# Optimization experiments

Measured on AMD Instinct MI355X. Metric: run time of the kernel, lower is better.

The kernel has to match this reference:

```python
import jax, jax.numpy as jnp
import numpy as np

N_NODES = 16384
N_EDGES = 98304
N_CAND = 1024
# GAT config from default __init__: heads=[8,8,1], features=[3,64,128,64]
LAYERS = [
    (3, 8, 64, True, True),      # (f_in, n_heads, f_out, concat, elu)
    (512, 8, 128, True, True),
    (1024, 1, 64, False, False),
]


def _gat_layer(x, src, tgt, W, a_src, a_tgt, b, skipW, nh, fo, concat, act):
    n = x.shape[0]
    proj = (x @ W).reshape(n, nh, fo)                 # [N, NH, F]
    s_src = jnp.einsum('nhf,hf->nh', proj, a_src)     # [N, NH]
    s_tgt = jnp.einsum('nhf,hf->nh', proj, a_tgt)
    e = jax.nn.leaky_relu(s_src[src] + s_tgt[tgt], 0.2)   # [E, NH]
    # numerically stable segment softmax over incoming edges of each target node
    e_max = jax.ops.segment_max(e, tgt, num_segments=n)
    ex = jnp.exp(e - jax.lax.stop_gradient(e_max)[tgt])
    denom = jax.ops.segment_sum(ex, tgt, num_segments=n)
    alpha = ex / (denom[tgt] + 1e-16)                 # [E, NH]
    agg = jax.ops.segment_sum(proj[src] * alpha[:, :, None], tgt, num_segments=n)
    out = agg + (x @ skipW).reshape(n, nh, fo)        # skip connection (projected)
    out = out.reshape(n, nh * fo) if concat else out.mean(axis=1)
    out = out + b
    return jax.nn.elu(out) if act else out


def setup_inputs() -> dict:
    key = jax.random.key(0)
    ks = iter(jax.random.split(key, 32))
    d = {}
    d['fea'] = jax.random.normal(next(ks), (N_NODES, 3), dtype=jnp.float32)
    d['edge_index'] = jax.random.randint(next(ks), (2, N_EDGES), 0, N_NODES, dtype=jnp.int32)
    d['candidates_id'] = jax.random.randint(next(ks), (N_CAND,), 0, N_NODES, dtype=jnp.int32)
    for i, (fi, nh, fo, concat, _) in enumerate(LAYERS):
        sc = 1.0 / np.sqrt(fi)
        d[f'W{i}'] = jax.random.normal(next(ks), (fi, nh * fo), dtype=jnp.float32) * sc
        d[f'a_src{i}'] = jax.random.normal(next(ks), (nh, fo), dtype=jnp.float32) * 0.1
        d[f'a_tgt{i}'] = jax.random.normal(next(ks), (nh, fo), dtype=jnp.float32) * 0.1
        d[f'b{i}'] = jnp.zeros((nh * fo if concat else fo,), dtype=jnp.float32)
        d[f'skip{i}'] = jax.random.normal(next(ks), (fi, nh * fo), dtype=jnp.float32) * sc
    # MLP head build_mlp(256, 3, 64, 1): 64->256 Tanh 256->256 Tanh 256->1
    for j, (a, bdim) in enumerate([(64, 256), (256, 256), (256, 1)], start=1):
        d[f'mW{j}'] = jax.random.normal(next(ks), (a, bdim), dtype=jnp.float32) / np.sqrt(a)
        d[f'mb{j}'] = jnp.zeros((bdim,), dtype=jnp.float32)
    return d


def reference(fea, edge_index, candidates_id,
              W0, a_src0, a_tgt0, b0, skip0,
              W1, a_src1, a_tgt1, b1, skip1,
              W2, a_src2, a_tgt2, b2, skip2,
              mW1, mb1, mW2, mb2, mW3, mb3):
    src, tgt = edge_index[0], edge_index[1]
    x = fea
    params = [(W0, a_src0, a_tgt0, b0, skip0), (W1, a_src1, a_tgt1, b1, skip1),
              (W2, a_src2, a_tgt2, b2, skip2)]
    for (fi, nh, fo, concat, act), (W, asr, atg, b, sk) in zip(LAYERS, params):
        x = _gat_layer(x, src, tgt, W, asr, atg, b, sk, nh, fo, concat, act)
    cand = x[candidates_id]                              # [C, 64]
    h = jnp.tanh(cand @ mW1 + mb1)
    h = jnp.tanh(h @ mW2 + mb2)
    prob = (h @ mW3 + mb3).squeeze(-1)                   # [C]
    return prob, candidates_id
```

## Files before the change

kernel.cpp:

```cpp
#include <hip/hip_runtime.h>
#include <cmath>

#define N_NODES 16384
#define N_EDGES 98304
#define N_CAND  1024

typedef __bf16 bf16x8 __attribute__((ext_vector_type(8)));
typedef short  s16x8  __attribute__((ext_vector_type(8)));
typedef float  f32x4  __attribute__((ext_vector_type(4)));
typedef unsigned short u16x2 __attribute__((ext_vector_type(2)));
typedef unsigned short u16x4 __attribute__((ext_vector_type(4)));

__device__ __forceinline__ unsigned short f2bf(float x) {
    unsigned u = __float_as_uint(x);
    return (unsigned short)((u + 0x7fffu + ((u >> 16) & 1u)) >> 16);
}
__device__ __forceinline__ float bf2f(unsigned short b) {
    return __uint_as_float((unsigned)b << 16);
}

#define GLL(gp, lp) __builtin_amdgcn_global_load_lds(                          \
    (const __attribute__((address_space(1))) unsigned int*)(const void*)(gp),  \
    (__attribute__((address_space(3))) unsigned int*)(void*)(lp), 16, 0, 0)

__global__ __launch_bounds__(256) void k_hist(const int* __restrict__ tgt,
                                              int* __restrict__ deg) {
    int e = blockIdx.x * 256 + threadIdx.x;
    if (e < N_EDGES) atomicAdd(&deg[tgt[e]], 1);
}

__global__ __launch_bounds__(256) void k_scan1(const int* __restrict__ deg,
                                               int* __restrict__ off,
                                               int* __restrict__ bsum) {
    __shared__ int s[256];
    int b = blockIdx.x, tid = threadIdx.x;
    int v = deg[b * 256 + tid];
    s[tid] = v;
    __syncthreads();
    for (int o = 1; o < 256; o <<= 1) {
        int t = (tid >= o) ? s[tid - o] : 0;
        __syncthreads();
        s[tid] += t;
        __syncthreads();
    }
    off[b * 256 + tid] = s[tid] - v;
    if (tid == 255) bsum[b] = s[255];
}

__global__ __launch_bounds__(64) void k_scan2(const int* __restrict__ bsum,
                                              int* __restrict__ bbase,
                                              int* __restrict__ off) {
    int tid = threadIdx.x;
    int v = bsum[tid];
    int x = v;
    #pragma unroll
    for (int o = 1; o < 64; o <<= 1) {
        int t = __shfl_up(x, o);
        if (tid >= o) x += t;
    }
    bbase[tid] = x - v;
    if (tid == 63) off[N_NODES] = x;
}

__global__ __launch_bounds__(256) void k_scan3(int* __restrict__ off,
                                               const int* __restrict__ bbase,
                                               int* __restrict__ cursor) {
    int i = blockIdx.x * 256 + threadIdx.x;
    int o = off[i] + bbase[blockIdx.x];
    off[i] = o;
    cursor[i] = o;
}

__global__ __launch_bounds__(256) void k_scatter(const int* __restrict__ ei,
                                                 int* __restrict__ cursor,
                                                 int* __restrict__ csrc) {
    int e = blockIdx.x * 256 + threadIdx.x;
    if (e < N_EDGES) {
        int s = ei[e];
        int t = ei[N_EDGES + e];
        int pos = atomicAdd(&cursor[t], 1);
        csrc[pos] = s;
    }
}

__global__ __launch_bounds__(256) void k_l0s(const float* __restrict__ fea,
                                             const float* __restrict__ W0,
                                             const float* __restrict__ as,
                                             const float* __restrict__ at,
                                             float* __restrict__ ssrc,
                                             float* __restrict__ stgt) {
    int n = blockIdx.x, tid = threadIdx.x;
    float f0 = fea[n * 3 + 0], f1 = fea[n * 3 + 1], f2 = fea[n * 3 + 2];
    int c1 = tid, c2 = tid + 256;
    float p1 = f0 * W0[c1] + f1 * W0[512 + c1] + f2 * W0[1024 + c1];
    float p2 = f0 * W0[c2] + f1 * W0[512 + c2] + f2 * W0[1024 + c2];
    float vs1 = p1 * as[c1], vt1 = p1 * at[c1];
    float vs2 = p2 * as[c2], vt2 = p2 * at[c2];
    #pragma unroll
    for (int o = 32; o; o >>= 1) {
        vs1 += __shfl_xor(vs1, o); vt1 += __shfl_xor(vt1, o);
        vs2 += __shfl_xor(vs2, o); vt2 += __shfl_xor(vt2, o);
    }
    int lane = tid & 63, w = tid >> 6;
    if (lane == 0) {
        ssrc[n * 8 + w]     = vs1;  stgt[n * 8 + w]     = vt1;
        ssrc[n * 8 + w + 4] = vs2;  stgt[n * 8 + w + 4] = vt2;
    }
}

template <int F, int NTOT>
__global__ __launch_bounds__(256) void k_pack(const float* __restrict__ src0,
                                              const float* __restrict__ src1,
                                              int splitN,
                                              unsigned short* __restrict__ hi,
                                              unsigned short* __restrict__ lo) {
    constexpr int NKB = F / 32;
    constexpr int TOT = (NTOT / 128) * NKB * 512;
    int s = blockIdx.x * 256 + threadIdx.x;
    if (s >= TOT) return;
    int nb = s / (NKB * 512);
    int rem = s - nb * (NKB * 512);
    int kb = rem >> 9;
    int sl = rem & 511;
    int c = sl >> 7, n = sl & 127;
    int col = nb * 128 + n;
    const float* src;
    int cc, stride;
    if (col < splitN) { src = src0; cc = col; stride = splitN; }
    else              { src = src1; cc = col - splitN; stride = NTOT - splitN; }
    int k0 = kb * 32 + c * 8;
    s16x8 hv, lv;
    #pragma unroll
    for (int j = 0; j < 8; ++j) {
        float w = src[(size_t)(k0 + j) * stride + cc];
        unsigned short h = f2bf(w);
        hv[j] = (short)h;
        lv[j] = (short)f2bf(w - bf2f(h));
    }
    *(s16x8*)(hi + (size_t)s * 8) = hv;
    *(s16x8*)(lo + (size_t)s * 8) = lv;
}

template <int F, int NTOT>
__global__ __launch_bounds__(256, 2) void k_gemm_mfma(
    const unsigned short* __restrict__ Xhi, const unsigned short* __restrict__ Xlo,
    const unsigned short* __restrict__ Wph, const unsigned short* __restrict__ Wpl,
    float* __restrict__ out0, float* __restrict__ out1, int splitN) {
    constexpr int NKB = F / 32;
    __shared__ unsigned short lds[2 * 16384];
    const int tid = threadIdx.x;
    const int bm  = blockIdx.y * 128;
    const int nb  = blockIdx.x;

    const int sA0 = tid, sA1 = tid + 256;
    const int rA0 = sA0 >> 2, rA1 = sA1 >> 2;
    const int cA0 = (sA0 & 3) ^ ((rA0 >> 1) & 3);
    const int cA1 = (sA1 & 3) ^ ((rA1 >> 1) & 3);
    const unsigned short* gAh0 = Xhi + (size_t)(bm + rA0) * F + cA0 * 8;
    const unsigned short* gAh1 = Xhi + (size_t)(bm + rA1) * F + cA1 * 8;
    const unsigned short* gAl0 = Xlo + (size_t)(bm + rA0) * F + cA0 * 8;
    const unsigned short* gAl1 = Xlo + (size_t)(bm + rA1) * F + cA1 * 8;
    const unsigned short* gBh  = Wph + (size_t)nb * NKB * 4096;
    const unsigned short* gBl  = Wpl + (size_t)nb * NKB * 4096;

    const int wave = tid >> 6, lane = tid & 63;
    const int wm = wave >> 1, wn = wave & 1;
    const int l15 = lane & 15, lc = lane >> 4;

    int offA[4], offB[4];
    #pragma unroll
    for (int mi = 0; mi < 4; ++mi) {
        int row = wm * 64 + mi * 16 + l15;
        int chp = lc ^ ((row >> 1) & 3);
        offA[mi] = row * 32 + chp * 8;
    }
    #pragma unroll
    for (int ni = 0; ni < 4; ++ni) {
        int n = wn * 64 + ni * 16 + l15;
        offB[ni] = 8192 + (lc * 128 + n) * 8;
    }

    f32x4 acc[4][4];
    #pragma unroll
    for (int i = 0; i < 4; ++i)
        #pragma unroll
        for (int j = 0; j < 4; ++j)
            acc[i][j] = (f32x4){0.f, 0.f, 0.f, 0.f};

    auto stage = [&](int kb, int buf) {
        unsigned short* l = &lds[buf * 16384];
        const size_t ka  = (size_t)kb * 32;
        const size_t kbb = (size_t)kb * 4096;
        GLL(gAh0 + ka, l + sA0 * 8);
        GLL(gAh1 + ka, l + sA1 * 8);
        GLL(gAl0 + ka, l + 4096 + sA0 * 8);
        GLL(gAl1 + ka, l + 4096 + sA1 * 8);
        GLL(gBh + kbb + sA0 * 8, l + 8192 + sA0 * 8);
        GLL(gBh + kbb + sA1 * 8, l + 8192 + sA1 * 8);
        GLL(gBl + kbb + sA0 * 8, l + 12288 + sA0 * 8);
        GLL(gBl + kbb + sA1 * 8, l + 12288 + sA1 * 8);
    };

    stage(0, 0);
    __syncthreads();

    for (int kb = 0; kb < NKB; ++kb) {
        const int buf = kb & 1;
        if (kb + 1 < NKB) stage(kb + 1, buf ^ 1);
        const unsigned short* l = &lds[buf * 16384];
        bf16x8 ah[4], al[4], bh[4], bl[4];
        #pragma unroll
        for (int mi = 0; mi < 4; ++mi) {
            ah[mi] = *(const bf16x8*)(l + offA[mi]);
            al[mi] = *(const bf16x8*)(l + 4096 + offA[mi]);
        }
        #pragma unroll
        for (int ni = 0; ni < 4; ++ni) {
            bh[ni] = *(const bf16x8*)(l + offB[ni]);
            bl[ni] = *(const bf16x8*)(l + 4096 + offB[ni]);
        }
        #pragma unroll
        for (int mi = 0; mi < 4; ++mi)
            #pragma unroll
            for (int ni = 0; ni < 4; ++ni) {
                acc[mi][ni] = __builtin_amdgcn_mfma_f32_16x16x32_bf16(ah[mi], bh[ni], acc[mi][ni], 0, 0, 0);
                acc[mi][ni] = __builtin_amdgcn_mfma_f32_16x16x32_bf16(ah[mi], bl[ni], acc[mi][ni], 0, 0, 0);
                acc[mi][ni] = __builtin_amdgcn_mfma_f32_16x16x32_bf16(al[mi], bh[ni], acc[mi][ni], 0, 0, 0);
            }
        __syncthreads();
    }

    #pragma unroll
    for (int ni = 0; ni < 4; ++ni) {
        int col = nb * 128 + wn * 64 + ni * 16 + l15;
        float* o;
        int cc, stride;
        if (col < splitN) { o = out0; cc = col; stride = splitN; }
        else              { o = out1; cc = col - splitN; stride = NTOT - splitN; }
        #pragma unroll
        for (int mi = 0; mi < 4; ++mi) {
            int row0 = bm + wm * 64 + mi * 16 + lc * 4;
            #pragma unroll
            for (int r = 0; r < 4; ++r)
                o[(size_t)(row0 + r) * stride + cc] = acc[mi][ni][r];
        }
    }
}

template <int H, int FO>
__global__ __launch_bounds__(256) void k_scores(const float* __restrict__ P,
                                                const float* __restrict__ asrc,
                                                const float* __restrict__ atgt,
                                                float* __restrict__ ssrc,
                                                float* __restrict__ stgt) {
    constexpr int K = H * FO;
    int gid  = blockIdx.x * 4 + (threadIdx.x >> 6);
    int lane = threadIdx.x & 63;
    int n = gid / H, h = gid - n * H;
    if (n >= N_NODES) return;
    float vs = 0.f, vt = 0.f;
    #pragma unroll
    for (int q = 0; q < FO / 64; ++q) {
        int f = lane + q * 64;
        float p = P[(size_t)n * K + h * FO + f];
        vs += p * asrc[h * FO + f];
        vt += p * atgt[h * FO + f];
    }
    #pragma unroll
    for (int o = 32; o; o >>= 1) {
        vs += __shfl_xor(vs, o);
        vt += __shfl_xor(vt, o);
    }
    if (lane == 0) {
        ssrc[n * H + h] = vs;
        stgt[n * H + h] = vt;
    }
}

__global__ __launch_bounds__(256) void k_attn0(
    const float* __restrict__ fea, const float* __restrict__ W0,
    const float* __restrict__ sk0, const float* __restrict__ ssrc,
    const float* __restrict__ stgt, const int* __restrict__ off,
    const int* __restrict__ csrc, const float* __restrict__ bias,
    unsigned short* __restrict__ ohi, unsigned short* __restrict__ olo) {
    constexpr int H = 8, K = 512;
    int n = blockIdx.x, tid = threadIdx.x;
    __shared__ float st[H], mh[H], dh[H];
    __shared__ int   srcs[256];
    __shared__ float sfea[256][3];
    __shared__ float av[256 * H];
    const int c0 = tid * 2, h0 = tid >> 5;

    float w00 = W0[c0],        w01 = W0[c0 + 1];
    float w10 = W0[512 + c0],  w11 = W0[512 + c0 + 1];
    float w20 = W0[1024 + c0], w21 = W0[1024 + c0 + 1];

    int d0 = off[n], deg = off[n + 1] - d0;
    if (tid < H) {
        st[tid] = stgt[n * H + tid];
        mh[tid] = -INFINITY;
        dh[tid] = 0.f;
    }
    __syncthreads();

    for (int base = 0; base < deg; base += 256) {
        int cnt = min(256, deg - base);
        if (tid < cnt) srcs[tid] = csrc[d0 + base + tid];
        __syncthreads();
        for (int idx = tid; idx < cnt * H; idx += 256) {
            int e = idx >> 3, h = idx & 7;
            float v = ssrc[srcs[e] * H + h] + st[h];
            av[idx] = (v >= 0.f) ? v : 0.2f * v;
        }
        __syncthreads();
        if (tid < H) {
            float m = mh[tid], d = dh[tid];
            float cm = -INFINITY;
            for (int e = 0; e < cnt; ++e) cm = fmaxf(cm, av[e * H + tid]);
            float nm = fmaxf(m, cm);
            float s = 0.f;
            for (int e = 0; e < cnt; ++e) s += expf(av[e * H + tid] - nm);
            d = ((m == -INFINITY) ? 0.f : d * expf(m - nm)) + s;
            mh[tid] = nm;
            dh[tid] = d;
        }
        __syncthreads();
    }
    if (tid < H) dh[tid] = 1.f / (dh[tid] + 1e-16f);
    __syncthreads();

    float a0 = 0.f, a1 = 0.f;
    for (int base = 0; base < deg; base += 256) {
        int cnt = min(256, deg - base);
        if (tid < cnt) srcs[tid] = csrc[d0 + base + tid];
        __syncthreads();
        for (int idx = tid; idx < cnt * 3; idx += 256)
            sfea[idx / 3][idx % 3] = fea[srcs[idx / 3] * 3 + idx % 3];
        for (int idx = tid; idx < cnt * H; idx += 256) {
            int e = idx >> 3, h = idx & 7;
            float v = ssrc[srcs[e] * H + h] + st[h];
            v = (v >= 0.f) ? v : 0.2f * v;
            av[idx] = expf(v - mh[h]) * dh[h];
        }
        __syncthreads();
        for (int e = 0; e < cnt; ++e) {
            float al = av[e * H + h0];
            float f0 = sfea[e][0], f1 = sfea[e][1], f2 = sfea[e][2];
            a0 += (f0 * w00 + f1 * w10 + f2 * w20) * al;
            a1 += (f0 * w01 + f1 * w11 + f2 * w21) * al;
        }
        __syncthreads();
    }

    float f0 = fea[n * 3], f1 = fea[n * 3 + 1], f2 = fea[n * 3 + 2];
    float r0 = a0 + f0 * sk0[c0]     + f1 * sk0[512 + c0]     + f2 * sk0[1024 + c0]     + bias[c0];
    float r1 = a1 + f0 * sk0[c0 + 1] + f1 * sk0[512 + c0 + 1] + f2 * sk0[1024 + c0 + 1] + bias[c0 + 1];
    r0 = (r0 > 0.f) ? r0 : expm1f(r0);
    r1 = (r1 > 0.f) ? r1 : expm1f(r1);
    u16x2 hv, lv;
    unsigned short hb0 = f2bf(r0); hv[0] = hb0; lv[0] = f2bf(r0 - bf2f(hb0));
    unsigned short hb1 = f2bf(r1); hv[1] = hb1; lv[1] = f2bf(r1 - bf2f(hb1));
    *(u16x2*)(ohi + (size_t)n * K + c0) = hv;
    *(u16x2*)(olo + (size_t)n * K + c0) = lv;
}

template <int H, int FO, bool ACT, bool SPLIT>
__global__ __launch_bounds__(256) void k_attn_g(
    const float* __restrict__ P, const float* __restrict__ ssrc,
    const float* __restrict__ stgt, const int* __restrict__ off,
    const int* __restrict__ csrc, const float* __restrict__ bias,
    const float* __restrict__ skipin, float* __restrict__ outf,
    unsigned short* __restrict__ ohi, unsigned short* __restrict__ olo) {
    constexpr int K   = H * FO;
    constexpr int VEC = (K / 256 >= 4) ? 4 : ((K / 256 >= 1) ? (K / 256) : 1);
    constexpr int NT  = K / VEC;
    int n = blockIdx.x, tid = threadIdx.x;
    __shared__ float st[H], mh[H], dh[H];
    __shared__ int   srcs[256];
    __shared__ float av[256 * H];

    const int c0 = (tid < NT ? tid : 0) * VEC;
    const int h0 = c0 / FO;
    const float* pc = P + c0;

    int d0 = off[n], deg = off[n + 1] - d0;
    if (tid < H) {
        st[tid] = stgt[n * H + tid];
        mh[tid] = -INFINITY;
        dh[tid] = 0.f;
    }
    __syncthreads();

    for (int base = 0; base < deg; base += 256) {
        int cnt = min(256, deg - base);
        if (tid < cnt) srcs[tid] = csrc[d0 + base + tid];
        __syncthreads();
        for (int idx = tid; idx < cnt * H; idx += 256) {
            int e = idx / H, h = idx - (idx / H) * H;
            float v = ssrc[srcs[e] * H + h] + st[h];
            av[idx] = (v >= 0.f) ? v : 0.2f * v;
        }
        __syncthreads();
        if (tid < H) {
            float m = mh[tid], d = dh[tid];
            float cm = -INFINITY;
            for (int e = 0; e < cnt; ++e) cm = fmaxf(cm, av[e * H + tid]);
            float nm = fmaxf(m, cm);
            float s = 0.f;
            for (int e = 0; e < cnt; ++e) s += expf(av[e * H + tid] - nm);
            d = ((m == -INFINITY) ? 0.f : d * expf(m - nm)) + s;
            mh[tid] = nm;
            dh[tid] = d;
        }
        __syncthreads();
    }
    if (tid < H) dh[tid] = 1.f / (dh[tid] + 1e-16f);
    __syncthreads();

    float acc[VEC];
    #pragma unroll
    for (int j = 0; j < VEC; ++j) acc[j] = 0.f;

    for (int base = 0; base < deg; base += 256) {
        int cnt = min(256, deg - base);
        if (tid < cnt) srcs[tid] = csrc[d0 + base + tid];
        __syncthreads();
        for (int idx = tid; idx < cnt * H; idx += 256) {
            int e = idx / H, h = idx - (idx / H) * H;
            float v = ssrc[srcs[e] * H + h] + st[h];
            v = (v >= 0.f) ? v : 0.2f * v;
            av[idx] = expf(v - mh[h]) * dh[h];
        }
        __syncthreads();
        if (NT == 256 || tid < NT) {
            for (int e = 0; e < cnt; ++e) {
                float a = av[e * H + h0];
                if constexpr (VEC == 4) {
                    const float4 v = *(const float4*)(pc + (size_t)srcs[e] * K);
                    acc[0] += v.x * a; acc[1] += v.y * a;
                    acc[2] += v.z * a; acc[3] += v.w * a;
                } else {
                    acc[0] += pc[(size_t)srcs[e] * K] * a;
                }
            }
        }
        __syncthreads();
    }

    if (NT == 256 || tid < NT) {
        float r[VEC];
        if constexpr (VEC == 4) {
            const float4 s4 = *(const float4*)(skipin + (size_t)n * K + c0);
            r[0] = acc[0] + s4.x; r[1] = acc[1] + s4.y;
            r[2] = acc[2] + s4.z; r[3] = acc[3] + s4.w;
        } else {
            r[0] = acc[0] + skipin[(size_t)n * K + c0];
        }
        #pragma unroll
        for (int j = 0; j < VEC; ++j) {
            r[j] += bias[c0 + j];
            if (ACT) r[j] = (r[j] > 0.f) ? r[j] : expm1f(r[j]);
        }
        if constexpr (SPLIT) {
            if constexpr (VEC == 4) {
                u16x4 hv, lv;
                #pragma unroll
                for (int j = 0; j < 4; ++j) {
                    unsigned short hb = f2bf(r[j]);
                    hv[j] = hb; lv[j] = f2bf(r[j] - bf2f(hb));
                }
                *(u16x4*)(ohi + (size_t)n * K + c0) = hv;
                *(u16x4*)(olo + (size_t)n * K + c0) = lv;
            } else {
                unsigned short hb = f2bf(r[0]);
                ohi[(size_t)n * K + c0] = hb;
                olo[(size_t)n * K + c0] = f2bf(r[0] - bf2f(hb));
            }
        } else {
            if constexpr (VEC == 4) {
                *(float4*)(outf + (size_t)n * K + c0) =
                    make_float4(r[0], r[1], r[2], r[3]);
            } else {
                outf[(size_t)n * K + c0] = r[0];
            }
        }
    }
}

__global__ __launch_bounds__(256) void k_mlp(const float* __restrict__ X3,
                                             const int* __restrict__ cid,
                                             const float* __restrict__ W1,
                                             const float* __restrict__ b1,
                                             const float* __restrict__ W2,
                                             const float* __restrict__ b2,
                                             const float* __restrict__ W3,
                                             const float* __restrict__ b3,
                                             float* __restrict__ out) {
    __shared__ float cf[64], h1[256], red[4];
    int c = blockIdx.x, tid = threadIdx.x;
    int id = cid[c];
    if (tid < 64) cf[tid] = X3[(size_t)id * 64 + tid];
    __syncthreads();
    float a = b1[tid];
    #pragma unroll 8
    for (int k = 0; k < 64; ++k) a += cf[k] * W1[k * 256 + tid];
    h1[tid] = tanhf(a);
    __syncthreads();
    float a2 = b2[tid];
    #pragma unroll 8
    for (int k = 0; k < 256; ++k) a2 += h1[k] * W2[k * 256 + tid];
    float v = tanhf(a2) * W3[tid];
    #pragma unroll
    for (int o = 32; o; o >>= 1) v += __shfl_xor(v, o);
    if ((tid & 63) == 0) red[tid >> 6] = v;
    __syncthreads();
    if (tid == 0) {
        out[c] = red[0] + red[1] + red[2] + red[3] + b3[0];
        out[N_CAND + c] = (float)id;
    }
}

extern "C" void kernel_launch(void* const* d_in, const int* in_sizes, int n_in,
                              void* d_out, int out_size, void* d_ws, size_t ws_size,
                              hipStream_t stream) {
    const float* fea  = (const float*)d_in[0];
    const int*   ei   = (const int*)d_in[1];
    const int*   cid  = (const int*)d_in[2];
    const float* W0   = (const float*)d_in[3];
    const float* as0  = (const float*)d_in[4];
    const float* at0  = (const float*)d_in[5];
    const float* b0   = (const float*)d_in[6];
    const float* sk0  = (const float*)d_in[7];
    const float* W1   = (const float*)d_in[8];
    const float* as1  = (const float*)d_in[9];
    const float* at1  = (const float*)d_in[10];
    const float* b1   = (const float*)d_in[11];
    const float* sk1  = (const float*)d_in[12];
    const float* W2   = (const float*)d_in[13];
    const float* as2  = (const float*)d_in[14];
    const float* at2  = (const float*)d_in[15];
    const float* b2   = (const float*)d_in[16];
    const float* sk2  = (const float*)d_in[17];
    const float* mW1  = (const float*)d_in[18];
    const float* mb1  = (const float*)d_in[19];
    const float* mW2  = (const float*)d_in[20];
    const float* mb2  = (const float*)d_in[21];
    const float* mW3  = (const float*)d_in[22];
    const float* mb3  = (const float*)d_in[23];

    char* w = (char*)d_ws;
    auto alloc = [&](size_t bytes) -> void* {
        void* p = (void*)w;
        w += (bytes + 255) & ~(size_t)255;
        return p;
    };
    int*   deg    = (int*)alloc((size_t)N_NODES * 4);
    int*   off    = (int*)alloc((size_t)(N_NODES + 1) * 4);
    int*   cursor = (int*)alloc((size_t)N_NODES * 4);
    int*   csrc   = (int*)alloc((size_t)N_EDGES * 4);
    int*   bsum   = (int*)alloc(64 * 4);
    int*   bbase  = (int*)alloc(64 * 4);
    float* ssrc   = (float*)alloc((size_t)N_NODES * 8 * 4);
    float* stgt   = (float*)alloc((size_t)N_NODES * 8 * 4);
    float* P      = (float*)alloc((size_t)N_NODES * 1024 * 4);
    float* S      = (float*)alloc((size_t)N_NODES * 1024 * 4);
    unsigned short* Xs = (unsigned short*)alloc((size_t)N_NODES * 1024 * 4);
    unsigned short* pw1h = (unsigned short*)alloc((size_t)512 * 2048 * 2);
    unsigned short* pw1l = (unsigned short*)alloc((size_t)512 * 2048 * 2);
    unsigned short* pw2h = (unsigned short*)alloc((size_t)1024 * 128 * 2);
    unsigned short* pw2l = (unsigned short*)alloc((size_t)1024 * 128 * 2);

    unsigned short* X1hi = Xs;
    unsigned short* X1lo = Xs + (size_t)N_NODES * 512;
    unsigned short* X2hi = Xs;
    unsigned short* X2lo = Xs + (size_t)N_NODES * 1024;
    float* X3 = P + (size_t)8 * 1024 * 1024;

    hipMemsetAsync(deg, 0, (size_t)N_NODES * 4, stream);
    k_hist<<<N_EDGES / 256, 256, 0, stream>>>(ei + N_EDGES, deg);
    k_scan1<<<N_NODES / 256, 256, 0, stream>>>(deg, off, bsum);
    k_scan2<<<1, 64, 0, stream>>>(bsum, bbase, off);
    k_scan3<<<N_NODES / 256, 256, 0, stream>>>(off, bbase, cursor);
    k_scatter<<<N_EDGES / 256, 256, 0, stream>>>(ei, cursor, csrc);

    k_pack<512, 2048><<<(16 * 16 * 512) / 256, 256, 0, stream>>>(W1, sk1, 1024, pw1h, pw1l);
    k_pack<1024, 128><<<(1 * 32 * 512) / 256, 256, 0, stream>>>(W2, sk2, 64, pw2h, pw2l);

    k_l0s<<<N_NODES, 256, 0, stream>>>(fea, W0, as0, at0, ssrc, stgt);
    k_attn0<<<N_NODES, 256, 0, stream>>>(fea, W0, sk0, ssrc, stgt, off, csrc,
                                         b0, X1hi, X1lo);

    {
        dim3 g(16, N_NODES / 128);
        k_gemm_mfma<512, 2048><<<g, 256, 0, stream>>>(X1hi, X1lo, pw1h, pw1l, P, S, 1024);
    }
    k_scores<8, 128><<<N_NODES * 8 / 4, 256, 0, stream>>>(P, as1, at1, ssrc, stgt);
    k_attn_g<8, 128, true, true><<<N_NODES, 256, 0, stream>>>(
        P, ssrc, stgt, off, csrc, b1, S, nullptr, X2hi, X2lo);

    {
        dim3 g(1, N_NODES / 128);
        k_gemm_mfma<1024, 128><<<g, 256, 0, stream>>>(X2hi, X2lo, pw2h, pw2l, P, S, 64);
    }
    k_scores<1, 64><<<N_NODES / 4, 256, 0, stream>>>(P, as2, at2, ssrc, stgt);
    k_attn_g<1, 64, false, false><<<N_NODES, 256, 0, stream>>>(
        P, ssrc, stgt, off, csrc, b2, S, X3, nullptr, nullptr);

    k_mlp<<<N_CAND, 256, 0, stream>>>(X3, cid, mW1, mb1, mW2, mb2, mW3, mb3,
                                      (float*)d_out);
}
```

Baseline: 490.7 us.

## Split-K layer-2 GEMM, fuse scan/pack kernels, single-pass softmax for small degrees

The final-layer GEMM (only 128 output columns, so 128 blocks) is split along K into 4 slices to fill more CUs. A new reduction kernel sums the partials and also computes the attention scores, replacing k_scores. The three scan kernels collapse into one single-block scan, and the two weight-pack kernels merge into one launch. The attention kernels get a fast path for degree <=256 that computes logits once and keeps them in LDS instead of recomputing gathers. Costs: extra partial-sum traffic (4x16384x128 floats) and a serial single-block scan.

```diff
diff --git a/kernel.cpp b/kernel.cpp
--- a/kernel.cpp
+++ b/kernel.cpp
@@ -29,46 +29,41 @@
     if (e < N_EDGES) atomicAdd(&deg[tgt[e]], 1);
 }
 
-__global__ __launch_bounds__(256) void k_scan1(const int* __restrict__ deg,
-                                               int* __restrict__ off,
-                                               int* __restrict__ bsum) {
-    __shared__ int s[256];
-    int b = blockIdx.x, tid = threadIdx.x;
-    int v = deg[b * 256 + tid];
-    s[tid] = v;
+__global__ __launch_bounds__(256) void k_scan_all(const int* __restrict__ deg,
+                                                  int* __restrict__ off,
+                                                  int* __restrict__ cursor) {
+    __shared__ int ts[256];
+    int tid = threadIdx.x;
+    const int4* d4 = (const int4*)(deg + tid * 64);
+    int s = 0;
+    #pragma unroll
+    for (int i = 0; i < 16; ++i) {
+        int4 v = d4[i];
+        s += v.x + v.y + v.z + v.w;
+    }
+    ts[tid] = s;
     __syncthreads();
     for (int o = 1; o < 256; o <<= 1) {
-        int t = (tid >= o) ? s[tid - o] : 0;
-        __syncthreads();
-        s[tid] += t;
-        __syncthreads();
-    }
-    off[b * 256 + tid] = s[tid] - v;
-    if (tid == 255) bsum[b] = s[255];
-}
-
-__global__ __launch_bounds__(64) void k_scan2(const int* __restrict__ bsum,
-                                              int* __restrict__ bbase,
-                                              int* __restrict__ off) {
-    int tid = threadIdx.x;
-    int v = bsum[tid];
-    int x = v;
-    #pragma unroll
-    for (int o = 1; o < 64; o <<= 1) {
-        int t = __shfl_up(x, o);
-        if (tid >= o) x += t;
-    }
-    bbase[tid] = x - v;
-    if (tid == 63) off[N_NODES] = x;
-}
-
-__global__ __launch_bounds__(256) void k_scan3(int* __restrict__ off,
-                                               const int* __restrict__ bbase,
-                                               int* __restrict__ cursor) {
-    int i = blockIdx.x * 256 + threadIdx.x;
-    int o = off[i] + bbase[blockIdx.x];
-    off[i] = o;
-    cursor[i] = o;
+        int t = (tid >= o) ? ts[tid - o] : 0;
+        __syncthreads();
+        ts[tid] += t;
+        __syncthreads();
+    }
+    int run = ts[tid] - s;
+    int4* o4 = (int4*)(off + tid * 64);
+    int4* c4 = (int4*)(cursor + tid * 64);
+    #pragma unroll
+    for (int i = 0; i < 16; ++i) {
+        int4 v = d4[i];
+        int4 ov;
+        ov.x = run; run += v.x;
+        ov.y = run; run += v.y;
+        ov.z = run; run += v.z;
+        ov.w = run; run += v.w;
+        o4[i] = ov;
+        c4[i] = ov;
+    }
+    if (tid == 255) off[N_NODES] = run;
 }
 
 __global__ __launch_bounds__(256) void k_scatter(const int* __restrict__ ei,
@@ -108,16 +103,11 @@
     }
 }
 
-template <int F, int NTOT>
-__global__ __launch_bounds__(256) void k_pack(const float* __restrict__ src0,
-                                              const float* __restrict__ src1,
-                                              int splitN,
-                                              unsigned short* __restrict__ hi,
-                                              unsigned short* __restrict__ lo) {
-    constexpr int NKB = F / 32;
-    constexpr int TOT = (NTOT / 128) * NKB * 512;
-    int s = blockIdx.x * 256 + threadIdx.x;
-    if (s >= TOT) return;
+__device__ __forceinline__ void pack_slot(const float* __restrict__ src0,
+                                          const float* __restrict__ src1,
+                                          int splitN, int NTOT, int NKB, int s,
+                                          unsigned short* __restrict__ hi,
+                                          unsigned short* __restrict__ lo) {
     int nb = s / (NKB * 512);
     int rem = s - nb * (NKB * 512);
     int kb = rem >> 9;
@@ -141,12 +131,27 @@
     *(s16x8*)(lo + (size_t)s * 8) = lv;
 }
 
-template <int F, int NTOT>
+__global__ __launch_bounds__(256) void k_pack_all(
+    const float* __restrict__ W1, const float* __restrict__ sk1,
+    unsigned short* __restrict__ pw1h, unsigned short* __restrict__ pw1l,
+    const float* __restrict__ W2, const float* __restrict__ sk2,
+    unsigned short* __restrict__ pw2h, unsigned short* __restrict__ pw2l) {
+    int s = blockIdx.x * 256 + threadIdx.x;
+    if (s < 131072) {
+        pack_slot(W1, sk1, 1024, 2048, 16, s, pw1h, pw1l);
+    } else {
+        int s2 = s - 131072;
+        if (s2 < 16384) pack_slot(W2, sk2, 64, 128, 32, s2, pw2h, pw2l);
+    }
+}
+
+template <int F, int NTOT, int KS>
 __global__ __launch_bounds__(256, 2) void k_gemm_mfma(
     const unsigned short* __restrict__ Xhi, const unsigned short* __restrict__ Xlo,
     const unsigned short* __restrict__ Wph, const unsigned short* __restrict__ Wpl,
     float* __restrict__ out0, float* __restrict__ out1, int splitN) {
     constexpr int NKB = F / 32;
+    static_assert(KS == 1 || NTOT == 128, "split-K assumes single col-block");
     __shared__ unsigned short lds[2 * 16384];
     const int tid = threadIdx.x;
     const int bm  = blockIdx.y * 128;
@@ -160,8 +165,8 @@
     const unsigned short* gAh1 = Xhi + (size_t)(bm + rA1) * F + cA1 * 8;
     const unsigned short* gAl0 = Xlo + (size_t)(bm + rA0) * F + cA0 * 8;
     const unsigned short* gAl1 = Xlo + (size_t)(bm + rA1) * F + cA1 * 8;
-    const unsigned short* gBh  = Wph + (size_t)nb * NKB * 4096;
-    const unsigned short* gBl  = Wpl + (size_t)nb * NKB * 4096;
+    const unsigned short* gBh  = Wph + (KS == 1 ? (size_t)nb * NKB * 4096 : 0);
+    const unsigned short* gBl  = Wpl + (KS == 1 ? (size_t)nb * NKB * 4096 : 0);
 
     const int wave = tid >> 6, lane = tid & 63;
     const int wm = wave >> 1, wn = wave & 1;
@@ -201,12 +206,15 @@
         GLL(gBl + kbb + sA1 * 8, l + 12288 + sA1 * 8);
     };
 
-    stage(0, 0);
+    const int kb0 = (KS > 1) ? nb * (NKB / KS) : 0;
+    const int kbN = (KS > 1) ? (NKB / KS) : NKB;
+
+    stage(kb0, 0);
     __syncthreads();
 
-    for (int kb = 0; kb < NKB; ++kb) {
-        const int buf = kb & 1;
-        if (kb + 1 < NKB) stage(kb + 1, buf ^ 1);
+    for (int ki = 0; ki < kbN; ++ki) {
+        const int buf = ki & 1;
+        if (ki + 1 < kbN) stage(kb0 + ki + 1, buf ^ 1);
         const unsigned short* l = &lds[buf * 16384];
         bf16x8 ah[4], al[4], bh[4], bl[4];
         #pragma unroll
@@ -230,20 +238,79 @@
         __syncthreads();
     }
 
-    #pragma unroll
-    for (int ni = 0; ni < 4; ++ni) {
-        int col = nb * 128 + wn * 64 + ni * 16 + l15;
-        float* o;
-        int cc, stride;
-        if (col < splitN) { o = out0; cc = col; stride = splitN; }
-        else              { o = out1; cc = col - splitN; stride = NTOT - splitN; }
-        #pragma unroll
-        for (int mi = 0; mi < 4; ++mi) {
-            int row0 = bm + wm * 64 + mi * 16 + lc * 4;
+    if constexpr (KS > 1) {
+        #pragma unroll
+        for (int ni = 0; ni < 4; ++ni) {
+            int col = wn * 64 + ni * 16 + l15;
             #pragma unroll
-            for (int r = 0; r < 4; ++r)
-                o[(size_t)(row0 + r) * stride + cc] = acc[mi][ni][r];
-        }
+            for (int mi = 0; mi < 4; ++mi) {
+                int row0 = bm + wm * 64 + mi * 16 + lc * 4;
+                #pragma unroll
+                for (int r = 0; r < 4; ++r)
+                    out0[((size_t)nb * N_NODES + row0 + r) * NTOT + col] = acc[mi][ni][r];
+            }
+        }
+    } else {
+        #pragma unroll
+        for (int ni = 0; ni < 4; ++ni) {
+            int col = nb * 128 + wn * 64 + ni * 16 + l15;
+            float* o;
+            int cc, stride;
+            if (col < splitN) { o = out0; cc = col; stride = splitN; }
+            else              { o = out1; cc = col - splitN; stride = NTOT - splitN; }
+            #pragma unroll
+            for (int mi = 0; mi < 4; ++mi) {
+                int row0 = bm + wm * 64 + mi * 16 + lc * 4;
+                #pragma unroll
+                for (int r = 0; r < 4; ++r)
+                    o[(size_t)(row0 + r) * stride + cc] = acc[mi][ni][r];
+            }
+        }
+    }
+}
+
+__global__ __launch_bounds__(256) void k_red2s(const float* __restrict__ part,
+                                               const float* __restrict__ as2,
+                                               const float* __restrict__ at2,
+                                               float* __restrict__ P2,
+                                               float* __restrict__ S2,
+                                               float* __restrict__ ssrc,
+                                               float* __restrict__ stgt) {
+    int tid = threadIdx.x;
+    int node = blockIdx.x * 16 + (tid >> 4);
+    int cg = tid & 15;
+    int c0 = cg * 8;
+    const float* p0 = part + (size_t)node * 128 + c0;
+    float v[8];
+    {
+        float4 a = *(const float4*)(p0);
+        float4 b = *(const float4*)(p0 + 4);
+        v[0]=a.x; v[1]=a.y; v[2]=a.z; v[3]=a.w; v[4]=b.x; v[5]=b.y; v[6]=b.z; v[7]=b.w;
+    }
+    #pragma unroll
+    for (int ks = 1; ks < 4; ++ks) {
+        const float* pk = p0 + (size_t)ks * N_NODES * 128;
+        float4 a = *(const float4*)(pk);
+        float4 b = *(const float4*)(pk + 4);
+        v[0]+=a.x; v[1]+=a.y; v[2]+=a.z; v[3]+=a.w; v[4]+=b.x; v[5]+=b.y; v[6]+=b.z; v[7]+=b.w;
+    }
+    if (cg < 8) {
+        float s = 0.f, t = 0.f;
+        #pragma unroll
+        for (int j = 0; j < 8; ++j) {
+            s += v[j] * as2[c0 + j];
+            t += v[j] * at2[c0 + j];
+        }
+        #pragma unroll
+        for (int o = 1; o < 8; o <<= 1) { s += __shfl_xor(s, o); t += __shfl_xor(t, o); }
+        float* d = P2 + (size_t)node * 64 + c0;
+        *(float4*)(d)     = make_float4(v[0], v[1], v[2], v[3]);
+        *(float4*)(d + 4) = make_float4(v[4], v[5], v[6], v[7]);
+        if (cg == 0) { ssrc[node] = s; stgt[node] = t; }
+    } else {
+        float* d = S2 + (size_t)node * 64 + (c0 - 64);
+        *(float4*)(d)     = make_float4(v[0], v[1], v[2], v[3]);
+        *(float4*)(d + 4) = make_float4(v[4], v[5], v[6], v[7]);
     }
 }
 
@@ -296,51 +363,35 @@
     float w20 = W0[1024 + c0], w21 = W0[1024 + c0 + 1];
 
     int d0 = off[n], deg = off[n + 1] - d0;
-    if (tid < H) {
-        st[tid] = stgt[n * H + tid];
-        mh[tid] = -INFINITY;
-        dh[tid] = 0.f;
-    }
+    if (tid < H) st[tid] = stgt[n * H + tid];
     __syncthreads();
 
-    for (int base = 0; base < deg; base += 256) {
-        int cnt = min(256, deg - base);
-        if (tid < cnt) srcs[tid] = csrc[d0 + base + tid];
-        __syncthreads();
-        for (int idx = tid; idx < cnt * H; idx += 256) {
-            int e = idx >> 3, h = idx & 7;
-            float v = ssrc[srcs[e] * H + h] + st[h];
-            av[idx] = (v >= 0.f) ? v : 0.2f * v;
-        }
-        __syncthreads();
-        if (tid < H) {
-            float m = mh[tid], d = dh[tid];
-            float cm = -INFINITY;
-            for (int e = 0; e < cnt; ++e) cm = fmaxf(cm, av[e * H + tid]);
-            float nm = fmaxf(m, cm);
-            float s = 0.f;
-            for (int e = 0; e < cnt; ++e) s += expf(av[e * H + tid] - nm);
-            d = ((m == -INFINITY) ? 0.f : d * expf(m - nm)) + s;
-            mh[tid] = nm;
-            dh[tid] = d;
-        }
-        __syncthreads();
-    }
-    if (tid < H) dh[tid] = 1.f / (dh[tid] + 1e-16f);
-    __syncthreads();
-
     float a0 = 0.f, a1 = 0.f;
-    for (int base = 0; base < deg; base += 256) {
-        int cnt = min(256, deg - base);
-        if (tid < cnt) srcs[tid] = csrc[d0 + base + tid];
+
+    if (deg <= 256) {
+        int cnt = deg;
+        if (tid < cnt) srcs[tid] = csrc[d0 + tid];
         __syncthreads();
         for (int idx = tid; idx < cnt * 3; idx += 256)
             sfea[idx / 3][idx % 3] = fea[srcs[idx / 3] * 3 + idx % 3];
         for (int idx = tid; idx < cnt * H; idx += 256) {
             int e = idx >> 3, h = idx & 7;
             float v = ssrc[srcs[e] * H + h] + st[h];
-            v = (v >= 0.f) ? v : 0.2f * v;
-            av[idx] = expf(v - mh[h]) * dh[h];
+            av[idx] = (v >= 0.f) ? v : 0.2f * v;
+        }
+        __syncthreads();
+        if (tid < H) {
+            float m = -INFINITY;
+            for (int e = 0; e < cnt; ++e) m = fmaxf(m, av[e * H + tid]);
+            float s = 0.f;
+            for (int e = 0; e < cnt; ++e) s += expf(av[e * H + tid] - m);
+            mh[tid] = m;
+            dh[tid] = 1.f / (s + 1e-16f);
+        }
+        __syncthreads();
+        for (int idx = tid; idx < cnt * H; idx += 256) {
+            int h = idx & 7;
+            av[idx] = expf(av[idx] - mh[h]) * dh[h];
         }
         __syncthreads();
         for (int e = 0; e < cnt; ++e) {
@@ -349,7 +400,55 @@
             a0 += (f0 * w00 + f1 * w10 + f2 * w20) * al;
             a1 += (f0 * w01 + f1 * w11 + f2 * w21) * al;
         }
-        __syncthreads();
+    } else {
+        if (tid < H) { mh[tid] = -INFINITY; dh[tid] = 0.f; }
+        __syncthreads();
+        for (int base = 0; base < deg; base += 256) {
+            int cnt = min(256, deg - base);
+            if (tid < cnt) srcs[tid] = csrc[d0 + base + tid];
+            __syncthreads();
+            for (int idx = tid; idx < cnt * H; idx += 256) {
+                int e = idx >> 3, h = idx & 7;
+                float v = ssrc[srcs[e] * H + h] + st[h];
+                av[idx] = (v >= 0.f) ? v : 0.2f * v;
+            }
+            __syncthreads();
+            if (tid < H) {
+                float m = mh[tid], d = dh[tid];
+                float cm = -INFINITY;
+                for (int e = 0; e < cnt; ++e) cm = fmaxf(cm, av[e * H + tid]);
+                float nm = fmaxf(m, cm);
+                float s = 0.f;
+                for (int e = 0; e < cnt; ++e) s += expf(av[e * H + tid] - nm);
+                d = ((m == -INFINITY) ? 0.f : d * expf(m - nm)) + s;
+                mh[tid] = nm;
+                dh[tid] = d;
+            }
+            __syncthreads();
+        }
+        if (tid < H) dh[tid] = 1.f / (dh[tid] + 1e-16f);
+        __syncthreads();
+        for (int base = 0; base < deg; base += 256) {
+            int cnt = min(256, deg - base);
+            if (tid < cnt) srcs[tid] = csrc[d0 + base + tid];
+            __syncthreads();
+            for (int idx = tid; idx < cnt * 3; idx += 256)
+                sfea[idx / 3][idx % 3] = fea[srcs[idx / 3] * 3 + idx % 3];
+            for (int idx = tid; idx < cnt * H; idx += 256) {
+                int e = idx >> 3, h = idx & 7;
+                float v = ssrc[srcs[e] * H + h] + st[h];
+                v = (v >= 0.f) ? v : 0.2f * v;
+                av[idx] = expf(v - mh[h]) * dh[h];
+            }
+            __syncthreads();
+            for (int e = 0; e < cnt; ++e) {
+                float al = av[e * H + h0];
+                float f0 = sfea[e][0], f1 = sfea[e][1], f2 = sfea[e][2];
+                a0 += (f0 * w00 + f1 * w10 + f2 * w20) * al;
+                a1 += (f0 * w01 + f1 * w11 + f2 * w21) * al;
+            }
+            __syncthreads();
+        }
     }
 
     float f0 = fea[n * 3], f1 = fea[n * 3 + 1], f2 = fea[n * 3 + 2];
@@ -384,16 +483,16 @@
     const float* pc = P + c0;
 
     int d0 = off[n], deg = off[n + 1] - d0;
-    if (tid < H) {
-        st[tid] = stgt[n * H + tid];
-        mh[tid] = -INFINITY;
-        dh[tid] = 0.f;
-    }
+    if (tid < H) st[tid] = stgt[n * H + tid];
     __syncthreads();
 
-    for (int base = 0; base < deg; base += 256) {
-        int cnt = min(256, deg - base);
-        if (tid < cnt) srcs[tid] = csrc[d0 + base + tid];
+    float acc[VEC];
+    #pragma unroll
+    for (int j = 0; j < VEC; ++j) acc[j] = 0.f;
+
+    if (deg <= 256) {
+        int cnt = deg;
+        if (tid < cnt) srcs[tid] = csrc[d0 + tid];
         __syncthreads();
         for (int idx = tid; idx < cnt * H; idx += 256) {
             int e = idx / H, h = idx - (idx / H) * H;
@@ -402,34 +501,17 @@
         }
         __syncthreads();
         if (tid < H) {
-            float m = mh[tid], d = dh[tid];
-            float cm = -INFINITY;
-            for (int e = 0; e < cnt; ++e) cm = fmaxf(cm, av[e * H + tid]);
-            float nm = fmaxf(m, cm);
+            float m = -INFINITY;
+            for (int e = 0; e < cnt; ++e) m = fmaxf(m, av[e * H + tid]);
             float s = 0.f;
-            for (int e = 0; e < cnt; ++e) s += expf(av[e * H + tid] - nm);
-            d = ((m == -INFINITY) ? 0.f : d * expf(m - nm)) + s;
-            mh[tid] = nm;
-            dh[tid] = d;
-        }
-        __syncthreads();
-    }
-    if (tid < H) dh[tid] = 1.f / (dh[tid] + 1e-16f);
-    __syncthreads();
-
-    float acc[VEC];
-    #pragma unroll
-    for (int j = 0; j < VEC; ++j) acc[j] = 0.f;
-
-    for (int base = 0; base < deg; base += 256) {
-        int cnt = min(256, deg - base);
-        if (tid < cnt) srcs[tid] = csrc[d0 + base + tid];
+            for (int e = 0; e < cnt; ++e) s += expf(av[e * H + tid] - m);
+            mh[tid] = m;
+            dh[tid] = 1.f / (s + 1e-16f);
+        }
         __syncthreads();
         for (int idx = tid; idx < cnt * H; idx += 256) {
-            int e = idx / H, h = idx - (idx / H) * H;
-            float v = ssrc[srcs[e] * H + h] + st[h];
-            v = (v >= 0.f) ? v : 0.2f * v;
-            av[idx] = expf(v - mh[h]) * dh[h];
+            int h = idx - (idx / H) * H;
+            av[idx] = expf(av[idx] - mh[h]) * dh[h];
         }
         __syncthreads();
         if (NT == 256 || tid < NT) {
@@ -444,7 +526,59 @@
                 }
             }
         }
-        __syncthreads();
+    } else {
+        if (tid < H) { mh[tid] = -INFINITY; dh[tid] = 0.f; }
+        __syncthreads();
+        for (int base = 0; base < deg; base += 256) {
+            int cnt = min(256, deg - base);
+            if (tid < cnt) srcs[tid] = csrc[d0 + base + tid];
+            __syncthreads();
+            for (int idx = tid; idx < cnt * H; idx += 256) {
+                int e = idx / H, h = idx - (idx / H) * H;
+                float v = ssrc[srcs[e] * H + h] + st[h];
+                av[idx] = (v >= 0.f) ? v : 0.2f * v;
+            }
+            __syncthreads();
+            if (tid < H) {
+                float m = mh[tid], d = dh[tid];
+                float cm = -INFINITY;
+                for (int e = 0; e < cnt; ++e) cm = fmaxf(cm, av[e * H + tid]);
+                float nm = fmaxf(m, cm);
+                float s = 0.f;
+                for (int e = 0; e < cnt; ++e) s += expf(av[e * H + tid] - nm);
+                d = ((m == -INFINITY) ? 0.f : d * expf(m - nm)) + s;
+                mh[tid] = nm;
+                dh[tid] = d;
+            }
+            __syncthreads();
+        }
+        if (tid < H) dh[tid] = 1.f / (dh[tid] + 1e-16f);
+        __syncthreads();
+        for (int base = 0; base < deg; base += 256) {
+            int cnt = min(256, deg - base);
+            if (tid < cnt) srcs[tid] = csrc[d0 + base + tid];
+            __syncthreads();
+            for (int idx = tid; idx < cnt * H; idx += 256) {
+                int e = idx / H, h = idx - (idx / H) * H;
+                float v = ssrc[srcs[e] * H + h] + st[h];
+                v = (v >= 0.f) ? v : 0.2f * v;
+                av[idx] = expf(v - mh[h]) * dh[h];
+            }
+            __syncthreads();
+            if (NT == 256 || tid < NT) {
+                for (int e = 0; e < cnt; ++e) {
+                    float a = av[e * H + h0];
+                    if constexpr (VEC == 4) {
+                        const float4 v = *(const float4*)(pc + (size_t)srcs[e] * K);
+                        acc[0] += v.x * a; acc[1] += v.y * a;
+                        acc[2] += v.z * a; acc[3] += v.w * a;
+                    } else {
+                        acc[0] += pc[(size_t)srcs[e] * K] * a;
+                    }
+                }
+            }
+            __syncthreads();
+        }
     }
 
     if (NT == 256 || tid < NT) {
@@ -558,8 +692,6 @@
     int*   off    = (int*)alloc((size_t)(N_NODES + 1) * 4);
     int*   cursor = (int*)alloc((size_t)N_NODES * 4);
     int*   csrc   = (int*)alloc((size_t)N_EDGES * 4);
-    int*   bsum   = (int*)alloc(64 * 4);
-    int*   bbase  = (int*)alloc(64 * 4);
     float* ssrc   = (float*)alloc((size_t)N_NODES * 8 * 4);
     float* stgt   = (float*)alloc((size_t)N_NODES * 8 * 4);
     float* P      = (float*)alloc((size_t)N_NODES * 1024 * 4);
@@ -574,17 +706,17 @@
     unsigned short* X1lo = Xs + (size_t)N_NODES * 512;
     unsigned short* X2hi = Xs;
     unsigned short* X2lo = Xs + (size_t)N_NODES * 1024;
-    float* X3 = P + (size_t)8 * 1024 * 1024;
+    float* part = P;
+    float* P2   = S;
+    float* S2   = S + (size_t)N_NODES * 64;
+    float* X3   = S + (size_t)2 * N_NODES * 64;
 
     hipMemsetAsync(deg, 0, (size_t)N_NODES * 4, stream);
     k_hist<<<N_EDGES / 256, 256, 0, stream>>>(ei + N_EDGES, deg);
-    k_scan1<<<N_NODES / 256, 256, 0, stream>>>(deg, off, bsum);
-    k_scan2<<<1, 64, 0, stream>>>(bsum, bbase, off);
-    k_scan3<<<N_NODES / 256, 256, 0, stream>>>(off, bbase, cursor);
+    k_scan_all<<<1, 256, 0, stream>>>(deg, off, cursor);
     k_scatter<<<N_EDGES / 256, 256, 0, stream>>>(ei, cursor, csrc);
 
-    k_pack<512, 2048><<<(16 * 16 * 512) / 256, 256, 0, stream>>>(W1, sk1, 1024, pw1h, pw1l);
-    k_pack<1024, 128><<<(1 * 32 * 512) / 256, 256, 0, stream>>>(W2, sk2, 64, pw2h, pw2l);
+    k_pack_all<<<576, 256, 0, stream>>>(W1, sk1, pw1h, pw1l, W2, sk2, pw2h, pw2l);
 
     k_l0s<<<N_NODES, 256, 0, stream>>>(fea, W0, as0, at0, ssrc, stgt);
     k_attn0<<<N_NODES, 256, 0, stream>>>(fea, W0, sk0, ssrc, stgt, off, csrc,
@@ -592,19 +724,19 @@
 
     {
         dim3 g(16, N_NODES / 128);
-        k_gemm_mfma<512, 2048><<<g, 256, 0, stream>>>(X1hi, X1lo, pw1h, pw1l, P, S, 1024);
+        k_gemm_mfma<512, 2048, 1><<<g, 256, 0, stream>>>(X1hi, X1lo, pw1h, pw1l, P, S, 1024);
     }
     k_scores<8, 128><<<N_NODES * 8 / 4, 256, 0, stream>>>(P, as1, at1, ssrc, stgt);
     k_attn_g<8, 128, true, true><<<N_NODES, 256, 0, stream>>>(
         P, ssrc, stgt, off, csrc, b1, S, nullptr, X2hi, X2lo);
 
     {
-        dim3 g(1, N_NODES / 128);
-        k_gemm_mfma<1024, 128><<<g, 256, 0, stream>>>(X2hi, X2lo, pw2h, pw2l, P, S, 64);
-    }
-    k_scores<1, 64><<<N_NODES / 4, 256, 0, stream>>>(P, as2, at2, ssrc, stgt);
+        dim3 g(4, N_NODES / 128);
+        k_gemm_mfma<1024, 128, 4><<<g, 256, 0, stream>>>(X2hi, X2lo, pw2h, pw2l, part, nullptr, 128);
+    }
+    k_red2s<<<N_NODES / 16, 256, 0, stream>>>(part, as2, at2, P2, S2, ssrc, stgt);
     k_attn_g<1, 64, false, false><<<N_NODES, 256, 0, stream>>>(
-        P, ssrc, stgt, off, csrc, b2, S, X3, nullptr, nullptr);
+        P2, ssrc, stgt, off, csrc, b2, S2, X3, nullptr, nullptr);
 
     k_mlp<<<N_CAND, 256, 0, stream>>>(X3, cid, mW1, mb1, mW2, mb2, mW3, mb3,
                                       (float*)d_out);
```

Result: faster. 468.4 us (-4.5%).
